# Kernel optimization log

Measured on AMD Instinct MI355X. Metric: run time of the kernel, lower is better.

## Reference

```python
import jax, jax.numpy as jnp
import numpy as np

EMBED = 1024
HEADS = 16
HEAD_DIM = EMBED // HEADS
RANK = 8
ALPHA = 16.0
SCALING = ALPHA / RANK  # 2.0
B, T = 2, 2048


def setup_inputs() -> dict:
    key = jax.random.key(0)
    ks = jax.random.split(key, 12)
    d = {
        'x': jax.random.normal(ks[0], (B, T, EMBED), dtype=jnp.float32),
        'Wq': jax.random.normal(ks[1], (EMBED, EMBED), dtype=jnp.float32),
        'Aq': jax.random.normal(ks[2], (EMBED, RANK), dtype=jnp.float32) * 0.01,
        'Bq': jnp.zeros((RANK, EMBED), dtype=jnp.float32),
        'Wk': jax.random.normal(ks[3], (EMBED, EMBED), dtype=jnp.float32),
        'Ak': jax.random.normal(ks[4], (EMBED, RANK), dtype=jnp.float32) * 0.01,
        'Bk': jnp.zeros((RANK, EMBED), dtype=jnp.float32),
        'Wv': jax.random.normal(ks[5], (EMBED, EMBED), dtype=jnp.float32),
        'Av': jax.random.normal(ks[6], (EMBED, RANK), dtype=jnp.float32) * 0.01,
        'Bv': jnp.zeros((RANK, EMBED), dtype=jnp.float32),
        'Wo': jax.random.normal(ks[7], (EMBED, EMBED), dtype=jnp.float32) * (1.0 / np.sqrt(EMBED)),
        'bo': jnp.zeros((EMBED,), dtype=jnp.float32),
    }
    return d


def _lora_linear(x, W, A, Bm):
    # torch F.linear(x, W) == x @ W.T ; LoRA bypass: x @ A @ B * scaling
    base = jnp.einsum('btc,oc->bto', x, W)
    lora = (x @ A) @ Bm * SCALING
    return base + lora


def reference(x, Wq, Aq, Bq, Wk, Ak, Bk, Wv, Av, Bv, Wo, bo):
    b, t, c = x.shape
    q = _lora_linear(x, Wq, Aq, Bq).reshape(b, t, HEADS, HEAD_DIM).transpose(0, 2, 1, 3)
    k = _lora_linear(x, Wk, Ak, Bk).reshape(b, t, HEADS, HEAD_DIM).transpose(0, 2, 1, 3)
    v = _lora_linear(x, Wv, Av, Bv).reshape(b, t, HEADS, HEAD_DIM).transpose(0, 2, 1, 3)
    scores = jnp.einsum('bhqd,bhkd->bhqk', q, k) / np.sqrt(HEAD_DIM).astype(np.float32)
    attn = jax.nn.softmax(scores, axis=-1)
    ctx = jnp.einsum('bhqk,bhkd->bhqd', attn, v)  # [B,H,T,D]
    out = ctx.transpose(0, 2, 1, 3).reshape(b, t, c)
    return jnp.einsum('btc,oc->bto', out, Wo) + bo
```

## Files before the change

kernel.cpp:

```cpp
#include <hip/hip_runtime.h>
#include <hip/hip_bf16.h>
#include <math.h>

#define EMBED 1024
#define HEADS 16
#define HDIM 64
#define RANK 8
#define BB 2
#define TT 2048
#define MTOT (BB*TT)
#define BH (BB*HEADS)

typedef __attribute__((ext_vector_type(8))) short bf16x8;
typedef __attribute__((ext_vector_type(4))) float f32x4;
typedef unsigned short u16;
typedef unsigned int u32;

__device__ __forceinline__ u16 f2bf(float f){
  unsigned u = __float_as_uint(f);
  u += 0x7FFF + ((u >> 16) & 1);
  return (u16)(u >> 16);
}
__device__ __forceinline__ float bf2f(u16 h){ return __uint_as_float(((unsigned)h) << 16); }

__device__ __forceinline__ u32 cvtpk(float lo, float hi){
  u32 r;
  asm("v_cvt_pk_bf16_f32 %0, %1, %2" : "=v"(r) : "v"(lo), "v"(hi));
  return r;
}

__device__ __forceinline__ void stage16(const void* g, void* l){
  __builtin_amdgcn_global_load_lds((const __attribute__((address_space(1))) unsigned int*)g,
                                   (__attribute__((address_space(3))) unsigned int*)l, 16, 0, 0);
}

__global__ void split_x_kernel(const float* __restrict__ x, u16* __restrict__ xhi, u16* __restrict__ xlo){
  int i = blockIdx.x * 256 + threadIdx.x;
  float v = x[i];
  u16 h = f2bf(v);
  xhi[i] = h;
  xlo[i] = f2bf(v - bf2f(h));
}

__global__ void prep_weights_kernel(const float* __restrict__ W0, const float* __restrict__ W1,
                                    const float* __restrict__ W2, const float* __restrict__ W3,
                                    const float* __restrict__ A0, const float* __restrict__ A1,
                                    const float* __restrict__ A2,
                                    const float* __restrict__ B0, const float* __restrict__ B1,
                                    const float* __restrict__ B2,
                                    u16* __restrict__ whi, u16* __restrict__ wlo,
                                    u16* __restrict__ wob){
  int i = blockIdx.x * 256 + threadIdx.x;
  int y = blockIdx.y;
  if (y == 3){ wob[i] = f2bf(W3[i]); return; }
  const float* W = (y == 0) ? W0 : (y == 1) ? W1 : W2;
  const float* A = (y == 0) ? A0 : (y == 1) ? A1 : A2;
  const float* Bm = (y == 0) ? B0 : (y == 1) ? B1 : B2;
  int o = i >> 10, c = i & 1023;
  float s = 0.f;
#pragma unroll
  for (int r = 0; r < RANK; ++r) s += A[c*RANK+r] * Bm[r*EMBED+o];
  float v = W[i] + 2.0f * s;
  u16 h = f2bf(v);
  size_t off = (size_t)y * 1048576 + i;
  whi[off] = h;
  wlo[off] = f2bf(v - bf2f(h));
}

__device__ __forceinline__ int swz4(int row){ return (row ^ (row >> 2)) & 3; }

__global__ __launch_bounds__(256)
void qkv_gemm(const u16* __restrict__ Ahi, const u16* __restrict__ Alo,
              const u16* __restrict__ Bhi, const u16* __restrict__ Blo,
              u16* __restrict__ qhi, u16* __restrict__ qlo,
              u16* __restrict__ khi, u16* __restrict__ klo,
              u16* __restrict__ vt)
{
  __shared__ __align__(16) u16 Ah[128*32], Bh[128*32], Al[128*32], Bl[128*32];
  const int t = threadIdx.x, lane = t & 63, w = t >> 6;
  const int wr = w >> 1, wc = w & 1;
  const int fr = lane & 15, fk = lane >> 4;
  const int m0 = blockIdx.y * 128, n0 = blockIdx.x * 128;
  const bool full = (n0 < 2048);

  f32x4 acc[4][4];
#pragma unroll
  for (int i = 0; i < 4; ++i)
#pragma unroll
    for (int j = 0; j < 4; ++j) acc[i][j] = (f32x4){0.f,0.f,0.f,0.f};

  for (int k0 = 0; k0 < EMBED; k0 += 32){
    __syncthreads();
#pragma unroll
    for (int cc = 0; cc < 2; ++cc){
      int cb = w*128 + cc*64;
      int chunk = cb + lane;
      int row = chunk >> 2, slot = chunk & 3;
      int sl = slot ^ swz4(row);
      stage16(Ahi + (size_t)(m0+row)*EMBED + k0 + sl*8, Ah + cb*8);
      stage16(Bhi + (size_t)(n0+row)*EMBED + k0 + sl*8, Bh + cb*8);
      if (full){
        stage16(Alo + (size_t)(m0+row)*EMBED + k0 + sl*8, Al + cb*8);
        stage16(Blo + (size_t)(n0+row)*EMBED + k0 + sl*8, Bl + cb*8);
      }
    }
    __syncthreads();

    bf16x8 ah[4], bh[4], al[4], bl[4];
#pragma unroll
    for (int i = 0; i < 4; ++i){
      int ra = wr*64 + i*16 + fr;
      int oa = ra*32 + (fk ^ swz4(ra))*8;
      ah[i] = *(const bf16x8*)&Ah[oa];
      if (full) al[i] = *(const bf16x8*)&Al[oa];
      int rb = wc*64 + i*16 + fr;
      int ob = rb*32 + (fk ^ swz4(rb))*8;
      bh[i] = *(const bf16x8*)&Bh[ob];
      if (full) bl[i] = *(const bf16x8*)&Bl[ob];
    }
#pragma unroll
    for (int i = 0; i < 4; ++i)
#pragma unroll
      for (int j = 0; j < 4; ++j){
        acc[i][j] = __builtin_amdgcn_mfma_f32_16x16x32_bf16(ah[i], bh[j], acc[i][j], 0,0,0);
        if (full){
          acc[i][j] = __builtin_amdgcn_mfma_f32_16x16x32_bf16(ah[i], bl[j], acc[i][j], 0,0,0);
          acc[i][j] = __builtin_amdgcn_mfma_f32_16x16x32_bf16(al[i], bh[j], acc[i][j], 0,0,0);
        }
      }
  }

  const int mat = (n0 + wc*64) >> 10;
  const float QSCALE = 0.125f * 1.44269504089f;
#pragma unroll
  for (int i = 0; i < 4; ++i)
#pragma unroll
    for (int j = 0; j < 4; ++j)
#pragma unroll
      for (int r = 0; r < 4; ++r){
        int gm = m0 + wr*64 + i*16 + fk*4 + r;
        int gn = n0 + wc*64 + j*16 + fr;
        int col = gn & 1023;
        float v = acc[i][j][r];
        int b = gm >> 11, tt2 = gm & 2047, h = col >> 6, d = col & 63;
        if (mat == 2){
          vt[((size_t)(b*HEADS + h)*HDIM + d)*TT + tt2] = f2bf(v);
        } else {
          if (mat == 0) v *= QSCALE;
          size_t idx = ((size_t)(b*HEADS + h)*TT + tt2)*HDIM + d;
          u16 hi = f2bf(v);
          u16 lo = f2bf(v - bf2f(hi));
          if (mat == 0){ qhi[idx] = hi; qlo[idx] = lo; }
          else         { khi[idx] = hi; klo[idx] = lo; }
        }
      }
}

__global__ __launch_bounds__(256)
void attn_mfma(const u16* __restrict__ Qhi, const u16* __restrict__ Qlo,
               const u16* __restrict__ Khi, const u16* __restrict__ Klo,
               const u16* __restrict__ Vt,  u16* __restrict__ ctx)
{
  __shared__ __align__(16) u16 smem[16384];
  u16* Kh = smem;
  u16* Kl = smem + 4096;
  u16* Vs = smem + 8192;
  u16* Ps = smem + 12288;
  const int t = threadIdx.x, lane = t & 63, w = t >> 6;
  const int fr = lane & 15, fk = lane >> 4;
  const int bh = blockIdx.y, q0 = blockIdx.x * 64;
  const size_t kbase = (size_t)bh * TT * HDIM;
  const size_t vbase = (size_t)bh * HDIM * TT;

#pragma unroll
  for (int cc = 0; cc < 2; ++cc){
    int cb = w*128 + cc*64;
    int chunk = cb + lane;
    int row = chunk >> 3, slot = chunk & 7;
    int sl = slot ^ (row & 7);
    stage16(Qhi + kbase + (size_t)(q0+row)*HDIM + sl*8, Kh + cb*8);
    stage16(Qlo + kbase + (size_t)(q0+row)*HDIM + sl*8, Kl + cb*8);
  }
  __syncthreads();
  bf16x8 qh[2], ql[2];
#pragma unroll
  for (int ks = 0; ks < 2; ++ks){
    int row = w*16 + fr;
    int off = row*64 + ((ks*4 + fk) ^ (row & 7))*8;
    qh[ks] = *(const bf16x8*)&Kh[off];
    ql[ks] = *(const bf16x8*)&Kl[off];
  }

  float mi = -1e30f, li = 0.f;
  f32x4 oacc[4];
#pragma unroll
  for (int n = 0; n < 4; ++n) oacc[n] = (f32x4){0.f,0.f,0.f,0.f};

  for (int kt = 0; kt < TT/64; ++kt){
    int kv0 = kt * 64;
    __syncthreads();
#pragma unroll
    for (int cc = 0; cc < 2; ++cc){
      int cb = w*128 + cc*64;
      int chunk = cb + lane;
      int row = chunk >> 3, slot = chunk & 7;
      int sl = slot ^ (row & 7);
      stage16(Khi + kbase + (size_t)(kv0+row)*HDIM + sl*8, Kh + cb*8);
      stage16(Klo + kbase + (size_t)(kv0+row)*HDIM + sl*8, Kl + cb*8);
      stage16(Vt  + vbase + (size_t)row*TT + kv0 + sl*8,  Vs + cb*8);
    }
    __syncthreads();

    f32x4 sacc[4];
#pragma unroll
    for (int n = 0; n < 4; ++n) sacc[n] = (f32x4){0.f,0.f,0.f,0.f};
#pragma unroll
    for (int n = 0; n < 4; ++n)
#pragma unroll
      for (int ks = 0; ks < 2; ++ks){
        int row = n*16 + fr;
        int off = row*64 + ((ks*4 + fk) ^ (row & 7))*8;
        bf16x8 kh = *(const bf16x8*)&Kh[off];
        bf16x8 kl = *(const bf16x8*)&Kl[off];
        sacc[n] = __builtin_amdgcn_mfma_f32_16x16x32_bf16(kh, qh[ks], sacc[n], 0,0,0);
        sacc[n] = __builtin_amdgcn_mfma_f32_16x16x32_bf16(kl, qh[ks], sacc[n], 0,0,0);
        sacc[n] = __builtin_amdgcn_mfma_f32_16x16x32_bf16(kh, ql[ks], sacc[n], 0,0,0);
      }

    float mt = fmaxf(fmaxf(sacc[0][0], sacc[0][1]), fmaxf(sacc[0][2], sacc[0][3]));
#pragma unroll
    for (int n = 1; n < 4; ++n)
      mt = fmaxf(mt, fmaxf(fmaxf(sacc[n][0], sacc[n][1]), fmaxf(sacc[n][2], sacc[n][3])));
    mt = fmaxf(mt, __shfl_xor(mt, 16));
    mt = fmaxf(mt, __shfl_xor(mt, 32));

    if (__any(mt > mi + 11.54f)){
      float mn = fmaxf(mi, mt);
      float sc = exp2f(mi - mn);
      mi = mn;
      li *= sc;
      float sct[4];
#pragma unroll
      for (int r = 0; r < 4; ++r) sct[r] = __shfl(sc, fk*4 + r);
#pragma unroll
      for (int n = 0; n < 4; ++n)
#pragma unroll
        for (int r = 0; r < 4; ++r) oacc[n][r] *= sct[r];
    }

    float rs = 0.f;
#pragma unroll
    for (int n = 0; n < 4; ++n)
#pragma unroll
      for (int r = 0; r < 4; ++r){
        float p = exp2f(sacc[n][r] - mi);
        sacc[n][r] = p;
        rs += p;
      }
    rs += __shfl_xor(rs, 16);
    rs += __shfl_xor(rs, 32);
    li += rs;

#pragma unroll
    for (int n = 0; n < 4; ++n){
      u32 u0 = cvtpk(sacc[n][0], sacc[n][1]);
      u32 u1 = cvtpk(sacc[n][2], sacc[n][3]);
      int slot = n*2 + (fk >> 1);
      int idx = w*1024 + fr*64 + (slot ^ (fr & 7))*8 + (fk & 1)*4;
      uint2 pk; pk.x = u0; pk.y = u1;
      *(uint2*)&Ps[idx] = pk;
    }

#pragma unroll
    for (int ks = 0; ks < 2; ++ks){
      bf16x8 pa = *(const bf16x8*)&Ps[w*1024 + fr*64 + ((ks*4 + fk) ^ (fr & 7))*8];
#pragma unroll
      for (int n = 0; n < 4; ++n){
        int row = n*16 + fr;
        bf16x8 bv = *(const bf16x8*)&Vs[row*64 + ((ks*4 + fk) ^ (row & 7))*8];
        oacc[n] = __builtin_amdgcn_mfma_f32_16x16x32_bf16(pa, bv, oacc[n], 0,0,0);
      }
    }
  }

  float inv = 1.f / li;
  float invt[4];
#pragma unroll
  for (int r = 0; r < 4; ++r) invt[r] = __shfl(inv, fk*4 + r);

  int b = bh >> 4, h = bh & 15;
#pragma unroll
  for (int r = 0; r < 4; ++r){
    int q = q0 + w*16 + fk*4 + r;
#pragma unroll
    for (int n = 0; n < 4; ++n){
      int d = n*16 + fr;
      ctx[((size_t)(b*TT + q))*EMBED + h*HDIM + d] = f2bf(oacc[n][r]*invt[r]);
    }
  }
}

__global__ __launch_bounds__(256)
void outproj_gemm(const u16* __restrict__ Ab, const u16* __restrict__ Bb,
                  const float* __restrict__ bias, float* __restrict__ C)
{
  __shared__ __align__(16) u16 Ah[128*32], Bh[128*32];
  const int t = threadIdx.x, lane = t & 63, w = t >> 6;
  const int wr = w >> 1, wc = w & 1;
  const int fr = lane & 15, fk = lane >> 4;
  const int m0 = blockIdx.y * 128, n0 = blockIdx.x * 128;

  f32x4 acc[4][4];
#pragma unroll
  for (int i = 0; i < 4; ++i)
#pragma unroll
    for (int j = 0; j < 4; ++j) acc[i][j] = (f32x4){0.f,0.f,0.f,0.f};

  for (int k0 = 0; k0 < EMBED; k0 += 32){
    __syncthreads();
#pragma unroll
    for (int cc = 0; cc < 2; ++cc){
      int cb = w*128 + cc*64;
      int chunk = cb + lane;
      int row = chunk >> 2, slot = chunk & 3;
      int sl = slot ^ swz4(row);
      stage16(Ab + (size_t)(m0+row)*EMBED + k0 + sl*8, Ah + cb*8);
      stage16(Bb + (size_t)(n0+row)*EMBED + k0 + sl*8, Bh + cb*8);
    }
    __syncthreads();

    bf16x8 ah[4], bh[4];
#pragma unroll
    for (int i = 0; i < 4; ++i){
      int ra = wr*64 + i*16 + fr;
      ah[i] = *(const bf16x8*)&Ah[ra*32 + (fk ^ swz4(ra))*8];
      int rb = wc*64 + i*16 + fr;
      bh[i] = *(const bf16x8*)&Bh[rb*32 + (fk ^ swz4(rb))*8];
    }
#pragma unroll
    for (int i = 0; i < 4; ++i)
#pragma unroll
      for (int j = 0; j < 4; ++j)
        acc[i][j] = __builtin_amdgcn_mfma_f32_16x16x32_bf16(ah[i], bh[j], acc[i][j], 0,0,0);
  }

#pragma unroll
  for (int i = 0; i < 4; ++i)
#pragma unroll
    for (int j = 0; j < 4; ++j)
#pragma unroll
      for (int r = 0; r < 4; ++r){
        int gm = m0 + wr*64 + i*16 + fk*4 + r;
        int gn = n0 + wc*64 + j*16 + fr;
        C[(size_t)gm*EMBED + gn] = acc[i][j][r] + bias[gn];
      }
}

extern "C" void kernel_launch(void* const* d_in, const int* in_sizes, int n_in,
                              void* d_out, int out_size, void* d_ws, size_t ws_size,
                              hipStream_t stream) {
  const float* x  = (const float*)d_in[0];
  const float* Wq = (const float*)d_in[1];
  const float* Aq = (const float*)d_in[2];
  const float* Bq = (const float*)d_in[3];
  const float* Wk = (const float*)d_in[4];
  const float* Ak = (const float*)d_in[5];
  const float* Bk = (const float*)d_in[6];
  const float* Wv = (const float*)d_in[7];
  const float* Av = (const float*)d_in[8];
  const float* Bv = (const float*)d_in[9];
  const float* Wo = (const float*)d_in[10];
  const float* bo = (const float*)d_in[11];
  float* out = (float*)d_out;

  char* ws = (char*)d_ws;
  const size_t MB = 1u << 20;
  u16* xhi  = (u16*)(ws + 0*MB);
  u16* xlo  = (u16*)(ws + 8*MB);
  u16* whi  = (u16*)(ws + 16*MB);
  u16* wlo  = (u16*)(ws + 22*MB);
  u16* wob  = (u16*)(ws + 28*MB);
  u16* qhi  = (u16*)(ws + 30*MB);
  u16* qlo  = (u16*)(ws + 38*MB);
  u16* khi  = (u16*)(ws + 46*MB);
  u16* klo  = (u16*)(ws + 54*MB);
  u16* vt   = (u16*)(ws + 62*MB);
  u16* ctx  = (u16*)(ws + 0*MB);

  dim3 blk(256);
  split_x_kernel<<<dim3(MTOT*EMBED/256), blk, 0, stream>>>(x, xhi, xlo);
  prep_weights_kernel<<<dim3(4096, 4), blk, 0, stream>>>(Wq, Wk, Wv, Wo, Aq, Ak, Av,
                                                         Bq, Bk, Bv, whi, wlo, wob);

  qkv_gemm<<<dim3(3*EMBED/128, MTOT/128), blk, 0, stream>>>(xhi, xlo, whi, wlo,
                                                            qhi, qlo, khi, klo, vt);

  attn_mfma<<<dim3(TT/64, BH), blk, 0, stream>>>(qhi, qlo, khi, klo, vt, ctx);

  outproj_gemm<<<dim3(EMBED/128, MTOT/128), blk, 0, stream>>>(ctx, wob, bo, out);
}
```

Baseline: 302.7 us.

## Register-prefetch next K/V tile and use raw v_exp_f32 in attention

```diff
diff --git a/kernel.cpp b/kernel.cpp
--- a/kernel.cpp
+++ b/kernel.cpp
@@ -26,6 +26,12 @@
 __device__ __forceinline__ u32 cvtpk(float lo, float hi){
   u32 r;
   asm("v_cvt_pk_bf16_f32 %0, %1, %2" : "=v"(r) : "v"(lo), "v"(hi));
+  return r;
+}
+
+__device__ __forceinline__ float fexp2(float x){
+  float r;
+  asm("v_exp_f32 %0, %1" : "=v"(r) : "v"(x));
   return r;
 }
 
@@ -181,6 +187,27 @@
     stage16(Qhi + kbase + (size_t)(q0+row)*HDIM + sl*8, Kh + cb*8);
     stage16(Qlo + kbase + (size_t)(q0+row)*HDIM + sl*8, Kl + cb*8);
   }
+
+  int dst[2];
+  const u16 *pKh[2], *pKl[2], *pV[2];
+#pragma unroll
+  for (int cc = 0; cc < 2; ++cc){
+    int chunk = w*128 + cc*64 + lane;
+    int row = chunk >> 3, slot = chunk & 7;
+    int sl = slot ^ (row & 7);
+    dst[cc] = chunk * 8;
+    pKh[cc] = Khi + kbase + (size_t)row*HDIM + sl*8;
+    pKl[cc] = Klo + kbase + (size_t)row*HDIM + sl*8;
+    pV [cc] = Vt  + vbase + (size_t)row*TT  + sl*8;
+  }
+  uint4 rKh[2], rKl[2], rV[2];
+#pragma unroll
+  for (int cc = 0; cc < 2; ++cc){
+    rKh[cc] = *(const uint4*)pKh[cc];  pKh[cc] += 64*HDIM;
+    rKl[cc] = *(const uint4*)pKl[cc];  pKl[cc] += 64*HDIM;
+    rV [cc] = *(const uint4*)pV [cc];  pV [cc] += 64;
+  }
+
   __syncthreads();
   bf16x8 qh[2], ql[2];
 #pragma unroll
@@ -197,19 +224,22 @@
   for (int n = 0; n < 4; ++n) oacc[n] = (f32x4){0.f,0.f,0.f,0.f};
 
   for (int kt = 0; kt < TT/64; ++kt){
-    int kv0 = kt * 64;
     __syncthreads();
 #pragma unroll
     for (int cc = 0; cc < 2; ++cc){
-      int cb = w*128 + cc*64;
-      int chunk = cb + lane;
-      int row = chunk >> 3, slot = chunk & 7;
-      int sl = slot ^ (row & 7);
-      stage16(Khi + kbase + (size_t)(kv0+row)*HDIM + sl*8, Kh + cb*8);
-      stage16(Klo + kbase + (size_t)(kv0+row)*HDIM + sl*8, Kl + cb*8);
-      stage16(Vt  + vbase + (size_t)row*TT + kv0 + sl*8,  Vs + cb*8);
-    }
-    __syncthreads();
+      *(uint4*)&Kh[dst[cc]] = rKh[cc];
+      *(uint4*)&Kl[dst[cc]] = rKl[cc];
+      *(uint4*)&Vs[dst[cc]] = rV[cc];
+    }
+    __syncthreads();
+    if (kt + 1 < TT/64){
+#pragma unroll
+      for (int cc = 0; cc < 2; ++cc){
+        rKh[cc] = *(const uint4*)pKh[cc];  pKh[cc] += 64*HDIM;
+        rKl[cc] = *(const uint4*)pKl[cc];  pKl[cc] += 64*HDIM;
+        rV [cc] = *(const uint4*)pV [cc];  pV [cc] += 64;
+      }
+    }
 
     f32x4 sacc[4];
 #pragma unroll
@@ -236,7 +266,7 @@
 
     if (__any(mt > mi + 11.54f)){
       float mn = fmaxf(mi, mt);
-      float sc = exp2f(mi - mn);
+      float sc = fexp2(mi - mn);
       mi = mn;
       li *= sc;
       float sct[4];
@@ -253,7 +283,7 @@
     for (int n = 0; n < 4; ++n)
 #pragma unroll
       for (int r = 0; r < 4; ++r){
-        float p = exp2f(sacc[n][r] - mi);
+        float p = fexp2(sacc[n][r] - mi);
         sacc[n][r] = p;
         rs += p;
       }
```

After: 424.1 us. 40.1% more time.
